# Performance work log

Measured on AMD Instinct MI355X. Metric: run time of the kernel, lower is better.

Reference implementation:

```python
import jax, jax.numpy as jnp
import numpy as np

NUM_NEIGHBORS = 3
EPS = 1e-10
B, N1, N2 = 8, 8192, 2048
C1, C2 = 256, 512


def setup_inputs() -> dict:
    key = jax.random.key(0)
    k1, k2, k3, k4 = jax.random.split(key, 4)
    return {
        "query_xyz": jax.random.uniform(k1, (B, 3, N1), dtype=jnp.float32),
        "key_xyz": jax.random.uniform(k2, (B, 3, N2), dtype=jnp.float32),
        "query_feature": jax.random.normal(k3, (B, C1, N1), dtype=jnp.float32),
        "key_feature": jax.random.normal(k4, (B, C2, N2), dtype=jnp.float32),
    }


def reference(query_xyz, key_xyz, query_feature, key_feature):
    # q: (B, N1, 3), k: (B, N2, 3)
    q = jnp.swapaxes(query_xyz, 1, 2)
    k = jnp.swapaxes(key_xyz, 1, 2)
    # squared pairwise distances (B, N1, N2) via ||q||^2 + ||k||^2 - 2 q.k
    d2 = (
        jnp.sum(q * q, axis=-1, keepdims=True)
        + jnp.sum(k * k, axis=-1)[:, None, :]
        - 2.0 * jnp.einsum("bnd,bmd->bnm", q, k)
    )
    # k nearest neighbors (smallest distances)
    neg_d, index = jax.lax.top_k(-d2, NUM_NEIGHBORS)  # (B, N1, K)
    distance = jnp.maximum(-neg_d, EPS)
    inv_distance = 1.0 / distance
    weight = inv_distance / jnp.sum(inv_distance, axis=2, keepdims=True)
    # torch.no_grad() block -> constants w.r.t. autodiff
    weight = jax.lax.stop_gradient(weight)
    index = jax.lax.stop_gradient(index)
    # gather key features: feat_t (B, N2, C2) -> gathered (B, N1, K, C2)
    feat_t = jnp.swapaxes(key_feature, 1, 2)
    batch_idx = jnp.arange(feat_t.shape[0])[:, None, None]
    gathered = feat_t[batch_idx, index]
    # inverse-distance weighted sum -> (B, C2, N1)
    interpolated = jnp.einsum("bnk,bnkc->bcn", weight, gathered)
    return jnp.concatenate([interpolated, query_feature], axis=1)
```

## Files before the change

kernel.cpp:

```cpp
#include <hip/hip_runtime.h>

#define NB 8
#define N1 8192
#define N2 2048
#define C1 256
#define C2 512
#define CO 768
#define CCH 4

typedef float f2 __attribute__((ext_vector_type(2)));
typedef float f4 __attribute__((ext_vector_type(4)));


#define NRM2(X, Y, Z) ({                                                   \
    float _s, _t;                                                          \
    asm("v_mul_f32 %0, %2, %2\n\t"                                         \
        "v_mul_f32 %1, %3, %3\n\t"                                         \
        "v_add_f32 %0, %0, %1\n\t"                                         \
        "v_mul_f32 %1, %4, %4\n\t"                                         \
        "v_add_f32 %0, %0, %1"                                             \
        : "=&v"(_s), "=&v"(_t) : "v"(X), "v"(Y), "v"(Z));                  \
    _s; })

#define PKD2(X01, Y01, Z01, K01, QXD, QYD, QZD, QQD, M2) ({                \
    f2 _d, _s;                                                             \
    asm("v_pk_mul_f32 %0, %2, %6\n\t"           \
        "v_pk_fma_f32 %0, %3, %7, %0\n\t"       \
        "v_pk_fma_f32 %0, %4, %8, %0\n\t"       \
        "v_pk_add_f32 %1, %5, %9\n\t"           \
        "v_pk_fma_f32 %0, %0, %10, %1"          \
        : "=&v"(_d), "=&v"(_s)                                             \
        : "v"(X01), "v"(Y01), "v"(Z01), "v"(K01),                          \
          "v"(QXD), "v"(QYD), "v"(QZD), "v"(QQD), "v"(M2));                \
    _d; })

#define INS(S, D2, J) do {                                                 \
        float _v = (D2);                                                   \
        bool c2 = _v < b2##S, c1 = _v < b1##S, c0 = _v < b0##S;            \
        i2##S = c2 ? (c1 ? i1##S : (J)) : i2##S;                           \
        b2##S = c2 ? (c1 ? b1##S : _v) : b2##S;                            \
        i1##S = c0 ? i0##S : (c1 ? (J) : i1##S);                           \
        b1##S = c0 ? b0##S : (c1 ? _v : b1##S);                            \
        i0##S = c0 ? (J) : i0##S;                                          \
        b0##S = c0 ? _v : b0##S;                                           \
    } while (0)

__global__ __launch_bounds__(512, 4) void knn_scan(
    const float* __restrict__ qxyz,
    const float* __restrict__ kxyz,
    const float* __restrict__ qfeat,
    int*   __restrict__ nn_idx,
    float* __restrict__ nn_w,
    float* __restrict__ out)
{
    __shared__ __align__(16) float skx[N2];
    __shared__ __align__(16) float sky[N2];
    __shared__ __align__(16) float skz[N2];
    __shared__ __align__(16) float skk[N2];
    __shared__ float pd[8][128][3];
    __shared__ int   pi[8][128][3];

    const int b    = blockIdx.x >> 6;
    const int tile = blockIdx.x & 63;
    const int n0   = tile * 128;
    const int tid  = threadIdx.x;
    const int w    = tid >> 6, lane = tid & 63;

    const float* kb = kxyz + (size_t)b * 3 * N2;
    for (int j = tid; j < N2; j += 512) {
        float x = kb[j], y = kb[N2 + j], z = kb[2 * N2 + j];
        skx[j] = x; sky[j] = y; skz[j] = z;
        skk[j] = NRM2(x, y, z);
    }
    __syncthreads();

    const int na = n0 + lane, nb = n0 + 64 + lane;
    const float* qb = qxyz + (size_t)b * 3 * N1;
    const float qxA = qb[na], qyA = qb[N1 + na], qzA = qb[2 * N1 + na];
    const float qxB = qb[nb], qyB = qb[N1 + nb], qzB = qb[2 * N1 + nb];
    const float qqA = NRM2(qxA, qyA, qzA);
    const float qqB = NRM2(qxB, qyB, qzB);

    f2 qxdA, qydA, qzdA, qqdA, qxdB, qydB, qzdB, qqdB, m2;
    qxdA.x = qxA; qxdA.y = qxA;  qydA.x = qyA; qydA.y = qyA;
    qzdA.x = qzA; qzdA.y = qzA;  qqdA.x = qqA; qqdA.y = qqA;
    qxdB.x = qxB; qxdB.y = qxB;  qydB.x = qyB; qydB.y = qyB;
    qzdB.x = qzB; qzdB.y = qzB;  qqdB.x = qqB; qqdB.y = qqB;
    m2.x = -2.0f; m2.y = -2.0f;

    float b0A = 3.4e38f, b1A = 3.4e38f, b2A = 3.4e38f;
    float b0B = 3.4e38f, b1B = 3.4e38f, b2B = 3.4e38f;
    int   i0A = 0, i1A = 0, i2A = 0, i0B = 0, i1B = 0, i2B = 0;

    const int jlo = w * (N2 / 8);
    #pragma unroll 4
    for (int g = 0; g < (N2 / 8) / 4; ++g) {
        const int jb = jlo + g * 4;
        f4 x4 = *(const f4*)&skx[jb];
        f4 y4 = *(const f4*)&sky[jb];
        f4 z4 = *(const f4*)&skz[jb];
        f4 k4 = *(const f4*)&skk[jb];
        f2 dA01 = PKD2(x4.xy, y4.xy, z4.xy, k4.xy, qxdA, qydA, qzdA, qqdA, m2);
        f2 dA23 = PKD2(x4.zw, y4.zw, z4.zw, k4.zw, qxdA, qydA, qzdA, qqdA, m2);
        f2 dB01 = PKD2(x4.xy, y4.xy, z4.xy, k4.xy, qxdB, qydB, qzdB, qqdB, m2);
        f2 dB23 = PKD2(x4.zw, y4.zw, z4.zw, k4.zw, qxdB, qydB, qzdB, qqdB, m2);
        INS(A, dA01.x, jb);     INS(A, dA01.y, jb + 1);
        INS(A, dA23.x, jb + 2); INS(A, dA23.y, jb + 3);
        INS(B, dB01.x, jb);     INS(B, dB01.y, jb + 1);
        INS(B, dB23.x, jb + 2); INS(B, dB23.y, jb + 3);
    }

    pd[w][lane][0] = b0A; pd[w][lane][1] = b1A; pd[w][lane][2] = b2A;
    pi[w][lane][0] = i0A; pi[w][lane][1] = i1A; pi[w][lane][2] = i2A;
    pd[w][64 + lane][0] = b0B; pd[w][64 + lane][1] = b1B; pd[w][64 + lane][2] = b2B;
    pi[w][64 + lane][0] = i0B; pi[w][64 + lane][1] = i1B; pi[w][64 + lane][2] = i2B;
    __syncthreads();

    if (tid < 128) {
        float m0 = 3.4e38f, m1 = 3.4e38f, m2s = 3.4e38f;
        int   j0 = 0, j1 = 0, j2 = 0;
        #pragma unroll
        for (int c = 0; c < 8; ++c) {
            #pragma unroll
            for (int s = 0; s < 3; ++s) {
                float d = pd[c][tid][s];
                int   i = pi[c][tid][s];
                if (d < m2s) {
                    bool c0 = d < m0, c1 = d < m1;
                    m2s = c1 ? m1 : d;               j2 = c1 ? j1 : i;
                    m1 = c0 ? m0 : (c1 ? d : m1);    j1 = c0 ? j0 : (c1 ? i : j1);
                    m0 = c0 ? d : m0;                j0 = c0 ? i  : j0;
                }
            }
        }
        float d0f = fmaxf(m0, 1e-10f), d1f = fmaxf(m1, 1e-10f), d2f = fmaxf(m2s, 1e-10f);
        float v0 = __fdiv_rn(1.0f, d0f), v1 = __fdiv_rn(1.0f, d1f), v2 = __fdiv_rn(1.0f, d2f);
        float s  = __fadd_rn(__fadd_rn(v0, v1), v2);
        const size_t g = (size_t)b * N1 + n0 + tid;
        *(int4*)  &nn_idx[g * 4] = make_int4(j0, j1, j2, 0);
        *(float4*)&nn_w  [g * 4] = make_float4(__fdiv_rn(v0, s), __fdiv_rn(v1, s),
                                               __fdiv_rn(v2, s), 0.0f);
    }

    const float4* qsrc = (const float4*)(qfeat + (size_t)b * C1 * N1);
    float4*       qdst = (float4*)(out + (size_t)b * CO * N1 + (size_t)C2 * N1);
    #pragma unroll
    for (int k = 0; k < 16; ++k) {
        const size_t r = (size_t)tile * 8192 + (size_t)k * 512 + tid;
        qdst[r] = qsrc[r];
    }
}

__global__ __launch_bounds__(256) void interp4(
    const float* __restrict__ kfeat,
    const int*   __restrict__ nn_idx,
    const float* __restrict__ nn_w,
    float* __restrict__ out)
{
    __shared__ __align__(16) float4 skf[N2];
    const int b     = blockIdx.x & 7;
    const int cg    = blockIdx.x >> 3;
    const int cbase = cg * CCH;
    const int tid   = threadIdx.x;

    const float* kf = kfeat + (size_t)b * C2 * N2 + (size_t)cbase * N2;
    for (int j = tid; j < N2; j += 256) {
        skf[j] = make_float4(kf[j], kf[N2 + j], kf[2 * N2 + j], kf[3 * N2 + j]);
    }
    __syncthreads();

    const int*   ib = nn_idx + (size_t)b * N1 * 4;
    const float* wb = nn_w   + (size_t)b * N1 * 4;
    float* ob = out + (size_t)b * CO * N1;

    #pragma unroll 4
    for (int t = 0; t < N1 / 256; ++t) {
        const int n = t * 256 + tid;
        const int4   iv = *(const int4*)  &ib[(size_t)n * 4];
        const float4 wv = *(const float4*)&wb[(size_t)n * 4];
        const float4 f0 = skf[iv.x];
        const float4 f1 = skf[iv.y];
        const float4 f2v = skf[iv.z];
        ob[(size_t)(cbase + 0) * N1 + n] =
            fmaf(wv.z, f2v.x, fmaf(wv.y, f1.x, __fmul_rn(wv.x, f0.x)));
        ob[(size_t)(cbase + 1) * N1 + n] =
            fmaf(wv.z, f2v.y, fmaf(wv.y, f1.y, __fmul_rn(wv.x, f0.y)));
        ob[(size_t)(cbase + 2) * N1 + n] =
            fmaf(wv.z, f2v.z, fmaf(wv.y, f1.z, __fmul_rn(wv.x, f0.z)));
        ob[(size_t)(cbase + 3) * N1 + n] =
            fmaf(wv.z, f2v.w, fmaf(wv.y, f1.w, __fmul_rn(wv.x, f0.w)));
    }
}

extern "C" void kernel_launch(void* const* d_in, const int* in_sizes, int n_in,
                              void* d_out, int out_size, void* d_ws, size_t ws_size,
                              hipStream_t stream) {
    const float* qxyz  = (const float*)d_in[0];
    const float* kxyz  = (const float*)d_in[1];
    const float* qfeat = (const float*)d_in[2];
    const float* kfeat = (const float*)d_in[3];
    float* out = (float*)d_out;

    int*   nn_idx = (int*)d_ws;
    float* nn_w   = (float*)d_ws + (size_t)4 * NB * N1;

    knn_scan<<<NB * (N1 / 128), 512, 0, stream>>>(qxyz, kxyz, qfeat,
                                                  nn_idx, nn_w, out);
    interp4<<<NB * (C2 / CCH), 256, 0, stream>>>(kfeat, nn_idx, nn_w, out);
}
```

Before: 117.6 us.

## Fuse kNN scan with interpolation using a transposed key-feature gather

Adds a pre-pass that transposes key features to (B, N2, C2) in workspace. A new fused kernel then does the kNN scan, keeps the neighbour indices and weights in shared memory, and gathers contiguous feature rows to interpolate a 128-point tile. It stages results in a shared tile so the output writes are coalesced. This removes the global round trip for indices and weights and the separate interpolation launch, but adds a 32 MB transpose write and read, plus gathers served from L2 instead of shared memory. It falls back to the old path when the workspace is too small.

```diff
diff --git a/kernel.cpp b/kernel.cpp
--- a/kernel.cpp
+++ b/kernel.cpp
@@ -45,13 +45,175 @@
         b0##S = c0 ? _v : b0##S;                                           \
     } while (0)
 
-__global__ __launch_bounds__(512, 4) void knn_scan(
+__global__ __launch_bounds__(256) void transpose_kf(
+    const float* __restrict__ kfeat,
+    float* __restrict__ ft)
+{
+    __shared__ float t[64][65];
+    const int jb = (blockIdx.x & 31) * 64;
+    const int cb = ((blockIdx.x >> 5) & 7) * 64;
+    const int b  = blockIdx.x >> 8;
+    const float* src = kfeat + (size_t)b * C2 * N2;
+    float* dst = ft + (size_t)b * N2 * C2;
+    const int lj = threadIdx.x & 63, hi = threadIdx.x >> 6;
+    #pragma unroll
+    for (int k = 0; k < 16; ++k) {
+        const int c = hi * 16 + k;
+        t[c][lj] = src[(size_t)(cb + c) * N2 + jb + lj];
+    }
+    __syncthreads();
+    #pragma unroll
+    for (int k = 0; k < 16; ++k) {
+        const int j = hi * 16 + k;
+        dst[(size_t)(jb + j) * C2 + cb + lj] = t[lj][j];
+    }
+}
+
+typedef float PdArr[128][3];
+typedef int   PiArr[128][3];
+
+__global__ __launch_bounds__(512, 4) void fused_all(
     const float* __restrict__ qxyz,
     const float* __restrict__ kxyz,
     const float* __restrict__ qfeat,
-    int*   __restrict__ nn_idx,
-    float* __restrict__ nn_w,
+    const float* __restrict__ ft,
     float* __restrict__ out)
+{
+    __shared__ __align__(16) char smem[128 * 131 * 4];
+    __shared__ int4   nni[128];
+    __shared__ float4 nnw[128];
+    float* skx = (float*)(smem);
+    float* sky = (float*)(smem + 8192);
+    float* skz = (float*)(smem + 16384);
+    float* skk = (float*)(smem + 24576);
+    PdArr* pd  = (PdArr*)(smem + 32768);
+    PiArr* pi  = (PiArr*)(smem + 45056);
+    float (*stile)[131] = (float(*)[131])smem;
+
+    const int b    = blockIdx.x & 7;
+    const int tile = blockIdx.x >> 3;
+    const int n0   = tile * 128;
+    const int tid  = threadIdx.x;
+    const int w    = tid >> 6, lane = tid & 63;
+
+    const float* kb = kxyz + (size_t)b * 3 * N2;
+    for (int j = tid; j < N2; j += 512) {
+        float x = kb[j], y = kb[N2 + j], z = kb[2 * N2 + j];
+        skx[j] = x; sky[j] = y; skz[j] = z;
+        skk[j] = NRM2(x, y, z);
+    }
+    __syncthreads();
+
+    const int na = n0 + lane, nb2 = n0 + 64 + lane;
+    const float* qb = qxyz + (size_t)b * 3 * N1;
+    const float qxA = qb[na], qyA = qb[N1 + na], qzA = qb[2 * N1 + na];
+    const float qxB = qb[nb2], qyB = qb[N1 + nb2], qzB = qb[2 * N1 + nb2];
+    const float qqA = NRM2(qxA, qyA, qzA);
+    const float qqB = NRM2(qxB, qyB, qzB);
+
+    f2 qxdA, qydA, qzdA, qqdA, qxdB, qydB, qzdB, qqdB, m2;
+    qxdA.x = qxA; qxdA.y = qxA;  qydA.x = qyA; qydA.y = qyA;
+    qzdA.x = qzA; qzdA.y = qzA;  qqdA.x = qqA; qqdA.y = qqA;
+    qxdB.x = qxB; qxdB.y = qxB;  qydB.x = qyB; qydB.y = qyB;
+    qzdB.x = qzB; qzdB.y = qzB;  qqdB.x = qqB; qqdB.y = qqB;
+    m2.x = -2.0f; m2.y = -2.0f;
+
+    float b0A = 3.4e38f, b1A = 3.4e38f, b2A = 3.4e38f;
+    float b0B = 3.4e38f, b1B = 3.4e38f, b2B = 3.4e38f;
+    int   i0A = 0, i1A = 0, i2A = 0, i0B = 0, i1B = 0, i2B = 0;
+
+    const int jlo = w * (N2 / 8);
+    #pragma unroll 4
+    for (int g = 0; g < (N2 / 8) / 4; ++g) {
+        const int jb = jlo + g * 4;
+        f4 x4 = *(const f4*)&skx[jb];
+        f4 y4 = *(const f4*)&sky[jb];
+        f4 z4 = *(const f4*)&skz[jb];
+        f4 k4 = *(const f4*)&skk[jb];
+        f2 dA01 = PKD2(x4.xy, y4.xy, z4.xy, k4.xy, qxdA, qydA, qzdA, qqdA, m2);
+        f2 dA23 = PKD2(x4.zw, y4.zw, z4.zw, k4.zw, qxdA, qydA, qzdA, qqdA, m2);
+        f2 dB01 = PKD2(x4.xy, y4.xy, z4.xy, k4.xy, qxdB, qydB, qzdB, qqdB, m2);
+        f2 dB23 = PKD2(x4.zw, y4.zw, z4.zw, k4.zw, qxdB, qydB, qzdB, qqdB, m2);
+        INS(A, dA01.x, jb);     INS(A, dA01.y, jb + 1);
+        INS(A, dA23.x, jb + 2); INS(A, dA23.y, jb + 3);
+        INS(B, dB01.x, jb);     INS(B, dB01.y, jb + 1);
+        INS(B, dB23.x, jb + 2); INS(B, dB23.y, jb + 3);
+    }
+
+    (*(pd + w))[lane][0] = b0A; (*(pd + w))[lane][1] = b1A; (*(pd + w))[lane][2] = b2A;
+    (*(pi + w))[lane][0] = i0A; (*(pi + w))[lane][1] = i1A; (*(pi + w))[lane][2] = i2A;
+    (*(pd + w))[64 + lane][0] = b0B; (*(pd + w))[64 + lane][1] = b1B; (*(pd + w))[64 + lane][2] = b2B;
+    (*(pi + w))[64 + lane][0] = i0B; (*(pi + w))[64 + lane][1] = i1B; (*(pi + w))[64 + lane][2] = i2B;
+    __syncthreads();
+
+    if (tid < 128) {
+        float m0 = 3.4e38f, m1 = 3.4e38f, m2s = 3.4e38f;
+        int   j0 = 0, j1 = 0, j2 = 0;
+        #pragma unroll
+        for (int c = 0; c < 8; ++c) {
+            #pragma unroll
+            for (int s = 0; s < 3; ++s) {
+                float d = (*(pd + c))[tid][s];
+                int   i = (*(pi + c))[tid][s];
+                if (d < m2s) {
+                    bool c0 = d < m0, c1 = d < m1;
+                    m2s = c1 ? m1 : d;               j2 = c1 ? j1 : i;
+                    m1 = c0 ? m0 : (c1 ? d : m1);    j1 = c0 ? j0 : (c1 ? i : j1);
+                    m0 = c0 ? d : m0;                j0 = c0 ? i  : j0;
+                }
+            }
+        }
+        float d0f = fmaxf(m0, 1e-10f), d1f = fmaxf(m1, 1e-10f), d2f = fmaxf(m2s, 1e-10f);
+        float v0 = __fdiv_rn(1.0f, d0f), v1 = __fdiv_rn(1.0f, d1f), v2 = __fdiv_rn(1.0f, d2f);
+        float s  = __fadd_rn(__fadd_rn(v0, v1), v2);
+        nni[tid] = make_int4(j0, j1, j2, 0);
+        nnw[tid] = make_float4(__fdiv_rn(v0, s), __fdiv_rn(v1, s),
+                               __fdiv_rn(v2, s), 0.0f);
+    }
+    __syncthreads();
+
+    const float* ftb = ft + (size_t)b * N2 * C2;
+    float* ob = out + (size_t)b * CO * N1;
+    #pragma unroll
+    for (int p = 0; p < 4; ++p) {
+        const int cbase = p * 128;
+        #pragma unroll 4
+        for (int qi = 0; qi < 16; ++qi) {
+            const int q = w * 16 + qi;
+            const int4   iv = nni[q];
+            const float4 wv = nnw[q];
+            #pragma unroll
+            for (int h = 0; h < 2; ++h) {
+                const int c = h * 64 + lane;
+                const float f0 = ftb[(size_t)iv.x * C2 + cbase + c];
+                const float f1 = ftb[(size_t)iv.y * C2 + cbase + c];
+                const float f2l = ftb[(size_t)iv.z * C2 + cbase + c];
+                stile[c][q] = fmaf(wv.z, f2l, fmaf(wv.y, f1, __fmul_rn(wv.x, f0)));
+            }
+        }
+        __syncthreads();
+        #pragma unroll
+        for (int it = 0; it < 32; ++it) {
+            const int idx = it * 512 + tid;
+            const int c = idx >> 7, q = idx & 127;
+            ob[(size_t)(cbase + c) * N1 + n0 + q] = stile[c][q];
+        }
+        __syncthreads();
+    }
+
+    const float4* qsrc = (const float4*)(qfeat + (size_t)b * C1 * N1);
+    float4*       qdst = (float4*)(out + (size_t)b * CO * N1 + (size_t)C2 * N1);
+    #pragma unroll
+    for (int k = 0; k < 16; ++k) {
+        const size_t r = (size_t)tile * 8192 + (size_t)k * 512 + tid;
+        qdst[r] = qsrc[r];
+    }
+}
+
+__global__ __launch_bounds__(512, 4) void knn_scan(
+    const float* __restrict__ qxyz, const float* __restrict__ kxyz,
+    const float* __restrict__ qfeat, int* __restrict__ nn_idx,
+    float* __restrict__ nn_w, float* __restrict__ out)
 {
     __shared__ __align__(16) float skx[N2];
     __shared__ __align__(16) float sky[N2];
@@ -74,10 +236,10 @@
     }
     __syncthreads();
 
-    const int na = n0 + lane, nb = n0 + 64 + lane;
+    const int na = n0 + lane, nb2 = n0 + 64 + lane;
     const float* qb = qxyz + (size_t)b * 3 * N1;
     const float qxA = qb[na], qyA = qb[N1 + na], qzA = qb[2 * N1 + na];
-    const float qxB = qb[nb], qyB = qb[N1 + nb], qzB = qb[2 * N1 + nb];
+    const float qxB = qb[nb2], qyB = qb[N1 + nb2], qzB = qb[2 * N1 + nb2];
     const float qqA = NRM2(qxA, qyA, qzA);
     const float qqB = NRM2(qxB, qyB, qzB);
 
@@ -152,10 +314,8 @@
 }
 
 __global__ __launch_bounds__(256) void interp4(
-    const float* __restrict__ kfeat,
-    const int*   __restrict__ nn_idx,
-    const float* __restrict__ nn_w,
-    float* __restrict__ out)
+    const float* __restrict__ kfeat, const int* __restrict__ nn_idx,
+    const float* __restrict__ nn_w, float* __restrict__ out)
 {
     __shared__ __align__(16) float4 skf[N2];
     const int b     = blockIdx.x & 7;
@@ -201,10 +361,16 @@
     const float* kfeat = (const float*)d_in[3];
     float* out = (float*)d_out;
 
-    int*   nn_idx = (int*)d_ws;
-    float* nn_w   = (float*)d_ws + (size_t)4 * NB * N1;
-
-    knn_scan<<<NB * (N1 / 128), 512, 0, stream>>>(qxyz, kxyz, qfeat,
-                                                  nn_idx, nn_w, out);
-    interp4<<<NB * (C2 / CCH), 256, 0, stream>>>(kfeat, nn_idx, nn_w, out);
-}
+    const size_t ft_bytes = (size_t)NB * N2 * C2 * 4;
+    if (ws_size >= ft_bytes) {
+        float* ft = (float*)d_ws;
+        transpose_kf<<<NB * 8 * 32, 256, 0, stream>>>(kfeat, ft);
+        fused_all<<<NB * (N1 / 128), 512, 0, stream>>>(qxyz, kxyz, qfeat, ft, out);
+    } else {
+        int*   nn_idx = (int*)d_ws;
+        float* nn_w   = (float*)d_ws + (size_t)4 * NB * N1;
+        knn_scan<<<NB * (N1 / 128), 512, 0, stream>>>(qxyz, kxyz, qfeat,
+                                                      nn_idx, nn_w, out);
+        interp4<<<NB * (C2 / CCH), 256, 0, stream>>>(kfeat, nn_idx, nn_w, out);
+    }
+}
```

New measurement: 130.1 us. +10.7%, slower.
